# Performance work log

Measured on AMD Instinct MI355X. Metric: run time of the kernel, lower is better.

The kernel has to match this reference:

```python
import jax, jax.numpy as jnp
import numpy as np

N = 100_000      # points
DEG = 16         # uniform neighbor count
E = N * DEG      # edges
NB = 4           # radial basis count (n)
MB = 4           # angular basis count (m)
FIN = 8
FOUT = 8
SUPPORT = 2.0    # module-level `support` constant in the original source


def _rbf_linear(nb, x, periodic):
    # evalRBFSeries(..., which='linear', epsilon=1.0): hat functions on [-1,1]
    if periodic:
        spacing = 2.0 / nb
        centroids = jnp.linspace(-1.0, 1.0, nb + 1)[:nb]          # [nb]
        ra = x[None, :] - centroids[:, None]                       # [nb, E]
        d = jnp.minimum(jnp.minimum(jnp.abs(ra), jnp.abs(ra - 2.0)), jnp.abs(ra + 2.0)) / spacing
    else:
        spacing = 2.0 / (nb - 1)
        centroids = jnp.linspace(-1.0, 1.0, nb)
        d = jnp.abs(x[None, :] - centroids[:, None]) / spacing     # [nb, E]
    return jnp.clip(1.0 - d, 0.0, 1.0)


def setup_inputs() -> dict:
    key = jax.random.key(0)
    k1, k2, k3, k4 = jax.random.split(key, 4)
    positions = jax.random.uniform(k1, (N, 2), dtype=jnp.float32)
    features = jax.random.normal(k2, (N, FIN), dtype=jnp.float32)
    # neighbors: DEG per point, never self (avoids zero-distance edges)
    offs = jax.random.randint(k3, (E,), 1, N)
    base = jnp.repeat(jnp.arange(N, dtype=jnp.int32), DEG)
    neighbors = ((base + offs) % N).astype(jnp.int32)
    row_splits = (jnp.arange(N + 1, dtype=jnp.int32) * DEG)
    # glorot_normal for kernel [fout, fin, n, m]
    kernel = jax.random.normal(k4, (FOUT, FIN, NB, MB), dtype=jnp.float32) * np.float32(
        np.sqrt(2.0 / ((FIN + FOUT) * NB * MB)))
    return {"positions": positions, "features": features, "kernel": kernel,
            "neighbors": neighbors, "row_splits": row_splits}


def reference(positions, features, kernel, neighbors, row_splits):
    n_pts = positions.shape[0]
    n_edges = neighbors.shape[0]
    counts = row_splits[1:] - row_splits[:-1]                       # [N]
    seg = jnp.repeat(jnp.arange(n_pts, dtype=jnp.int32), counts,
                     total_repeat_length=n_edges)                   # [E] owning point per edge
    rel = positions[neighbors] - positions[seg]                     # [E, 2]
    r = jnp.linalg.norm(rel, axis=1) / SUPPORT                      # [E]
    theta = jnp.arctan2(rel[:, 1], rel[:, 0])                       # [E]
    c = _rbf_linear(NB, r * 2.0 - 1.0, periodic=False)              # [NB, E]
    f = _rbf_linear(MB, theta / np.float32(np.pi), periodic=True)   # [MB, E]
    M = jnp.einsum('un,vn->nuv', c, f)                              # [E, NB, MB] per-edge outer product
    O = jnp.einsum('unm,ijnm->uij', M, kernel)                      # [E, FOUT, FIN]
    fv = features[neighbors]                                        # [E, FIN]
    FO = jnp.einsum('nij,nj->ni', O, fv)                            # [E, FOUT]
    return jax.ops.segment_sum(FO, seg, num_segments=n_pts)         # [N, FOUT]
```

## Files before the change

kernel.cpp:

```cpp
#include <hip/hip_runtime.h>
#include <hip/hip_fp16.h>
#include <math.h>


#define TWO_OVER_PI 0.63661977236758134f

typedef float v2f __attribute__((ext_vector_type(2)));

__device__ __forceinline__ float fast_atan2f(float y, float x) {
    float ax = fabsf(x), ay = fabsf(y);
    float mx = fmaxf(ax, ay);
    float mn = fminf(ax, ay);
    mx = fmaxf(mx, 1e-30f);
    float r = mn * __builtin_amdgcn_rcpf(mx);
    float s = r * r;
    float p = -0.0117212f;
    p = fmaf(p, s,  0.05265332f);
    p = fmaf(p, s, -0.11643287f);
    p = fmaf(p, s,  0.19354346f);
    p = fmaf(p, s, -0.33262347f);
    p = fmaf(p, s,  0.99997726f);
    float a = p * r;
    a = (ay > ax) ? (1.57079632679f - a) : a;
    a = (x < 0.0f) ? (3.14159265359f - a) : a;
    return copysignf(a, y);
}

__device__ __forceinline__ void edge_basis(float dx, float dy,
                                           float c[4], float f[4]) {
    float dist = sqrtf(fmaf(dx, dx, dy * dy));
    float tr = dist * 1.5f;
    float theta = fast_atan2f(dy, dx);
    float ta = fmaf(theta, TWO_OVER_PI, 2.0f);
#pragma unroll
    for (int n = 0; n < 4; ++n)
        c[n] = fmaxf(1.0f - fabsf(tr - (float)n), 0.0f);
#pragma unroll
    for (int m = 0; m < 4; ++m) {
        float d = fabsf(ta - (float)m);
        d = fminf(d, 4.0f - d);
        f[m] = fmaxf(1.0f - d, 0.0f);
    }
}

__device__ __forceinline__ float2 h2f(float bits) {
    union { float f; __half2 h; } u;
    u.f = bits;
    return make_float2(__low2float(u.h), __high2float(u.h));
}

__device__ __forceinline__ float h2f_pack(float a, float b) {
    union { __half2 h; float f; } u;
    u.h = __floats2half2_rn(a, b);
    return u.f;
}

__global__ __launch_bounds__(256) void pack_kernel(
    const float* __restrict__ positions,
    const float* __restrict__ features,
    float4*      __restrict__ packed,
    int npts)
{
    int u = blockIdx.x * blockDim.x + threadIdx.x;
    if (u >= npts) return;
    float2 p  = ((const float2*)positions)[u];
    float4 fa = ((const float4*)features)[u * 2];
    float4 fb = ((const float4*)features)[u * 2 + 1];
    float4 q0, q1;
    q0.x = p.x;
    q0.y = p.y;
    q0.z = h2f_pack(fa.x, fa.y);
    q0.w = h2f_pack(fa.z, fa.w);
    q1.x = p.x;
    q1.y = p.y;
    q1.z = h2f_pack(fb.x, fb.y);
    q1.w = h2f_pack(fb.z, fb.w);
    packed[u * 2]     = q0;
    packed[u * 2 + 1] = q1;
}

__global__ __launch_bounds__(256) void rbf_packed_kernel(
    const float* __restrict__ positions,
    const float4* __restrict__ packed,
    const float* __restrict__ kern,
    const int*   __restrict__ neighbors,
    const int*   __restrict__ row_splits,
    float*       __restrict__ out,
    int npts)
{
    __shared__ float Kl[1024];
    {
        const float4* src = (const float4*)kern;
        float4* dst = (float4*)Kl;
        dst[threadIdx.x] = src[threadIdx.x];
    }
    __syncthreads();

    int gt   = blockIdx.x * blockDim.x + threadIdx.x;
    int u    = gt >> 2;
    int sub  = gt & 3;
    int half = sub & 1;
    int eh   = sub >> 1;
    if (u >= npts) return;

    float2 pu = ((const float2*)positions)[u];
    int rs0 = row_splits[u];
    int rs1 = row_splits[u + 1];
    int cnt = rs1 - rs0;

    v2f g2[4][8];
#pragma unroll
    for (int j = 0; j < 4; ++j)
#pragma unroll
        for (int p = 0; p < 8; ++p) g2[j][p] = (v2f){0.0f, 0.0f};

#define VISIT(R)                                                              \
    {                                                                         \
        float c[4], f[4];                                                     \
        edge_basis(R.x - pu.x, R.y - pu.y, c, f);                             \
        v2f f2[2] = { {f[0], f[1]}, {f[2], f[3]} };                           \
        float2 lo = h2f(R.z);                                                 \
        float2 hi = h2f(R.w);                                                 \
        float fvj[4] = {lo.x, lo.y, hi.x, hi.y};                              \
        _Pragma("unroll")                                                     \
        for (int n = 0; n < 4; ++n) {                                         \
            _Pragma("unroll")                                                 \
            for (int mh = 0; mh < 2; ++mh) {                                  \
                v2f w2 = c[n] * f2[mh];                         \
                _Pragma("unroll")                                             \
                for (int j = 0; j < 4; ++j) {                                 \
                    v2f fb = { fvj[j], fvj[j] };                              \
                    g2[j][n * 2 + mh] =                                       \
                        __builtin_elementwise_fma(w2, fb, g2[j][n * 2 + mh]); \
                }                                                             \
            }                                                                 \
        }                                                                     \
    }

    if (cnt == 16) {
        int e0 = rs0 + eh * 8;
        const int4* nb4 = (const int4*)(neighbors + e0);
        int4 nA = nb4[0];
        int4 nB = nb4[1];

        float4 R0 = packed[nA.x * 2 + half];
        float4 R1 = packed[nA.y * 2 + half];
        float4 R2 = packed[nA.z * 2 + half];
        float4 R3 = packed[nA.w * 2 + half];
        float4 R4 = packed[nB.x * 2 + half];
        float4 R5 = packed[nB.y * 2 + half];
        float4 R6 = packed[nB.z * 2 + half];
        float4 R7 = packed[nB.w * 2 + half];

        VISIT(R0)
        VISIT(R1)
        VISIT(R2)
        VISIT(R3)
        VISIT(R4)
        VISIT(R5)
        VISIT(R6)
        VISIT(R7)
    } else {
        int c0 = (cnt + 1) >> 1;
        int e0 = rs0 + eh * c0;
        int e1 = (eh == 0) ? (rs0 + c0) : rs1;
        for (int e = e0; e < e1; ++e) {
            int nb = neighbors[e];
            float4 R = packed[nb * 2 + half];
            VISIT(R)
        }
    }
#undef VISIT

    float o[8];
    const float4* K4 = (const float4*)Kl;
#pragma unroll
    for (int i = 0; i < 8; ++i) {
        v2f acc = (v2f){0.0f, 0.0f};
#pragma unroll
        for (int j = 0; j < 4; ++j) {
            int jg = half * 4 + j;
            int base4 = (i * 128 + jg * 16) >> 2;
#pragma unroll
            for (int q = 0; q < 4; ++q) {
                float4 kv = K4[base4 + q];
                v2f klo = { kv.x, kv.y };
                v2f khi = { kv.z, kv.w };
                acc = __builtin_elementwise_fma(klo, g2[j][2 * q],     acc);
                acc = __builtin_elementwise_fma(khi, g2[j][2 * q + 1], acc);
            }
        }
        o[i] = acc.x + acc.y;
    }

#pragma unroll
    for (int i = 0; i < 8; ++i) {
        o[i] += __shfl_xor(o[i], 1);
        o[i] += __shfl_xor(o[i], 2);
    }

    float2 ov = (sub == 0) ? make_float2(o[0], o[1])
              : (sub == 1) ? make_float2(o[2], o[3])
              : (sub == 2) ? make_float2(o[4], o[5])
                           : make_float2(o[6], o[7]);
    ((float2*)out)[u * 4 + sub] = ov;
}

__global__ __launch_bounds__(256) void rbf_direct_kernel(
    const float* __restrict__ positions,
    const float* __restrict__ features,
    const float* __restrict__ kern,
    const int*   __restrict__ neighbors,
    const int*   __restrict__ row_splits,
    float*       __restrict__ out,
    int npts)
{
    __shared__ float Kl[1024];
    {
        const float4* src = (const float4*)kern;
        float4* dst = (float4*)Kl;
        dst[threadIdx.x] = src[threadIdx.x];
    }
    __syncthreads();

    int gt   = blockIdx.x * blockDim.x + threadIdx.x;
    int u    = gt >> 2;
    int sub  = gt & 3;
    int half = sub & 1;
    int eh   = sub >> 1;
    if (u >= npts) return;

    float2 pu = ((const float2*)positions)[u];
    int rs0 = row_splits[u];
    int rs1 = row_splits[u + 1];
    int cnt = rs1 - rs0;

    float g[16][4];
#pragma unroll
    for (int nm = 0; nm < 16; ++nm)
#pragma unroll
        for (int j = 0; j < 4; ++j) g[nm][j] = 0.0f;

    const float2* pos2  = (const float2*)positions;
    const float4* feat4 = (const float4*)features;

    int c0 = (cnt + 1) >> 1;
    int e0 = rs0 + eh * c0;
    int e1 = (eh == 0) ? (rs0 + c0) : rs1;
    for (int e = e0; e < e1; ++e) {
        int nb = neighbors[e];
        float2 pn = pos2[nb];
        float c[4], f[4];
        edge_basis(pn.x - pu.x, pn.y - pu.y, c, f);
        float4 fv = feat4[nb * 2 + half];
        float fvj[4] = {fv.x, fv.y, fv.z, fv.w};
#pragma unroll
        for (int n = 0; n < 4; ++n)
#pragma unroll
            for (int m = 0; m < 4; ++m) {
                float w = c[n] * f[m];
#pragma unroll
                for (int j = 0; j < 4; ++j)
                    g[n * 4 + m][j] = fmaf(w, fvj[j], g[n * 4 + m][j]);
            }
    }

    float o[8];
#pragma unroll
    for (int i = 0; i < 8; ++i) o[i] = 0.0f;
    const float4* K4 = (const float4*)Kl;
#pragma unroll
    for (int i = 0; i < 8; ++i) {
#pragma unroll
        for (int j = 0; j < 4; ++j) {
            int jg = half * 4 + j;
            int base4 = (i * 128 + jg * 16) >> 2;
#pragma unroll
            for (int q = 0; q < 4; ++q) {
                float4 kv = K4[base4 + q];
                o[i] = fmaf(kv.x, g[q * 4 + 0][j], o[i]);
                o[i] = fmaf(kv.y, g[q * 4 + 1][j], o[i]);
                o[i] = fmaf(kv.z, g[q * 4 + 2][j], o[i]);
                o[i] = fmaf(kv.w, g[q * 4 + 3][j], o[i]);
            }
        }
    }
#pragma unroll
    for (int i = 0; i < 8; ++i) {
        o[i] += __shfl_xor(o[i], 1);
        o[i] += __shfl_xor(o[i], 2);
    }
    float2 ov = (sub == 0) ? make_float2(o[0], o[1])
              : (sub == 1) ? make_float2(o[2], o[3])
              : (sub == 2) ? make_float2(o[4], o[5])
                           : make_float2(o[6], o[7]);
    ((float2*)out)[u * 4 + sub] = ov;
}

extern "C" void kernel_launch(void* const* d_in, const int* in_sizes, int n_in,
                              void* d_out, int out_size, void* d_ws, size_t ws_size,
                              hipStream_t stream) {
    const float* positions  = (const float*)d_in[0];
    const float* features   = (const float*)d_in[1];
    const float* kern       = (const float*)d_in[2];
    const int*   neighbors  = (const int*)d_in[3];
    const int*   row_splits = (const int*)d_in[4];
    float* out = (float*)d_out;

    int npts = in_sizes[0] / 2;
    int total = npts * 4;
    int block = 256;
    int grid = (total + block - 1) / block;

    size_t need = (size_t)npts * 32;
    if (ws_size >= need) {
        int pgrid = (npts + block - 1) / block;
        pack_kernel<<<pgrid, block, 0, stream>>>(positions, features,
                                                 (float4*)d_ws, npts);
        rbf_packed_kernel<<<grid, block, 0, stream>>>(positions,
                                                      (const float4*)d_ws, kern,
                                                      neighbors, row_splits,
                                                      out, npts);
    } else {
        rbf_direct_kernel<<<grid, block, 0, stream>>>(positions, features, kern,
                                                      neighbors, row_splits,
                                                      out, npts);
    }
}
```

Measured before the change: 91.51 us.

## Split each point across eight threads and reduce basis accumulators via shuffles

The packed kernel now gives each point eight lanes instead of four. Each lane visits four edges and handles one half of the features, and the launch bounds now request higher occupancy. Before the kernel contraction, the per-lane g2 accumulators are summed across the edge-quarter lanes with xor shuffles. Each lane then computes only two output channels, so the contraction work is split instead of done redundantly. This raises parallelism and cuts per-thread latency, but it adds 64 shuffles per lane and doubles the thread count.

```diff
diff --git a/kernel.cpp b/kernel.cpp
--- a/kernel.cpp
+++ b/kernel.cpp
@@ -53,6 +53,13 @@
     union { __half2 h; float f; } u;
     u.h = __floats2half2_rn(a, b);
     return u.f;
+}
+
+__device__ __forceinline__ v2f shfl_xor_v2(v2f v, int mask) {
+    v2f r;
+    r.x = __shfl_xor(v.x, mask);
+    r.y = __shfl_xor(v.y, mask);
+    return r;
 }
 
 __global__ __launch_bounds__(256) void pack_kernel(
@@ -79,7 +86,7 @@
     packed[u * 2 + 1] = q1;
 }
 
-__global__ __launch_bounds__(256) void rbf_packed_kernel(
+__global__ __launch_bounds__(256, 8) void rbf_packed_kernel(
     const float* __restrict__ positions,
     const float4* __restrict__ packed,
     const float* __restrict__ kern,
@@ -97,8 +104,8 @@
     __syncthreads();
 
     int gt   = blockIdx.x * blockDim.x + threadIdx.x;
-    int u    = gt >> 2;
-    int sub  = gt & 3;
+    int u    = gt >> 3;
+    int sub  = gt & 7;
     int half = sub & 1;
     int eh   = sub >> 1;
     if (u >= npts) return;
@@ -138,32 +145,21 @@
     }
 
     if (cnt == 16) {
-        int e0 = rs0 + eh * 8;
-        const int4* nb4 = (const int4*)(neighbors + e0);
-        int4 nA = nb4[0];
-        int4 nB = nb4[1];
-
-        float4 R0 = packed[nA.x * 2 + half];
-        float4 R1 = packed[nA.y * 2 + half];
-        float4 R2 = packed[nA.z * 2 + half];
-        float4 R3 = packed[nA.w * 2 + half];
-        float4 R4 = packed[nB.x * 2 + half];
-        float4 R5 = packed[nB.y * 2 + half];
-        float4 R6 = packed[nB.z * 2 + half];
-        float4 R7 = packed[nB.w * 2 + half];
-
+        int e0 = rs0 + eh * 4;
+        int4 nb = *(const int4*)(neighbors + e0);
+        float4 R0 = packed[nb.x * 2 + half];
+        float4 R1 = packed[nb.y * 2 + half];
+        float4 R2 = packed[nb.z * 2 + half];
+        float4 R3 = packed[nb.w * 2 + half];
         VISIT(R0)
         VISIT(R1)
         VISIT(R2)
         VISIT(R3)
-        VISIT(R4)
-        VISIT(R5)
-        VISIT(R6)
-        VISIT(R7)
     } else {
-        int c0 = (cnt + 1) >> 1;
-        int e0 = rs0 + eh * c0;
-        int e1 = (eh == 0) ? (rs0 + c0) : rs1;
+        int cq = (cnt + 3) >> 2;
+        int e0 = rs0 + eh * cq;
+        int e1 = e0 + cq;
+        if (e1 > rs1) e1 = rs1;
         for (int e = e0; e < e1; ++e) {
             int nb = neighbors[e];
             float4 R = packed[nb * 2 + half];
@@ -172,10 +168,20 @@
     }
 #undef VISIT
 
-    float o[8];
+#pragma unroll
+    for (int j = 0; j < 4; ++j)
+#pragma unroll
+        for (int p = 0; p < 8; ++p) {
+            g2[j][p] += shfl_xor_v2(g2[j][p], 2);
+            g2[j][p] += shfl_xor_v2(g2[j][p], 4);
+        }
+
+    int i0 = eh * 2;
     const float4* K4 = (const float4*)Kl;
-#pragma unroll
-    for (int i = 0; i < 8; ++i) {
+    float o[2];
+#pragma unroll
+    for (int t = 0; t < 2; ++t) {
+        int i = i0 + t;
         v2f acc = (v2f){0.0f, 0.0f};
 #pragma unroll
         for (int j = 0; j < 4; ++j) {
@@ -190,20 +196,13 @@
                 acc = __builtin_elementwise_fma(khi, g2[j][2 * q + 1], acc);
             }
         }
-        o[i] = acc.x + acc.y;
-    }
-
-#pragma unroll
-    for (int i = 0; i < 8; ++i) {
-        o[i] += __shfl_xor(o[i], 1);
-        o[i] += __shfl_xor(o[i], 2);
-    }
-
-    float2 ov = (sub == 0) ? make_float2(o[0], o[1])
-              : (sub == 1) ? make_float2(o[2], o[3])
-              : (sub == 2) ? make_float2(o[4], o[5])
-                           : make_float2(o[6], o[7]);
-    ((float2*)out)[u * 4 + sub] = ov;
+        o[t] = acc.x + acc.y;
+    }
+
+    o[0] += __shfl_xor(o[0], 1);
+    o[1] += __shfl_xor(o[1], 1);
+    if (half == 0)
+        ((float2*)out)[u * 4 + eh] = make_float2(o[0], o[1]);
 }
 
 __global__ __launch_bounds__(256) void rbf_direct_kernel(
@@ -308,20 +307,22 @@
     float* out = (float*)d_out;
 
     int npts = in_sizes[0] / 2;
-    int total = npts * 4;
     int block = 256;
-    int grid = (total + block - 1) / block;
 
     size_t need = (size_t)npts * 32;
     if (ws_size >= need) {
         int pgrid = (npts + block - 1) / block;
         pack_kernel<<<pgrid, block, 0, stream>>>(positions, features,
                                                  (float4*)d_ws, npts);
+        int total = npts * 8;
+        int grid = (total + block - 1) / block;
         rbf_packed_kernel<<<grid, block, 0, stream>>>(positions,
                                                       (const float4*)d_ws, kern,
                                                       neighbors, row_splits,
                                                       out, npts);
     } else {
+        int total = npts * 4;
+        int grid = (total + block - 1) / block;
         rbf_direct_kernel<<<grid, block, 0, stream>>>(positions, features, kern,
                                                       neighbors, row_splits,
                                                       out, npts);
```

After: 230.8 us. 2.52x slower.
